# Optimization experiments

Hardware: AMD Instinct MI355X
Metric: run time of the kernel (lower is better)

The kernel has to match this reference:

```python
import jax, jax.numpy as jnp
import numpy as np

EMB_DIM = 128
HEAD_SIZE = 16  # embDim // numHea = 128 // 8


def setup_inputs() -> dict:
    key = jax.random.key(0)
    k1, k2, k3, k4 = jax.random.split(key, 4)
    B, T = 8, 2048
    inpEmb = jax.random.normal(k1, (B, T, EMB_DIM), dtype=jnp.float32)
    # nn.Linear(embDim, heaSiz, bias=False) weights, stored transposed so y = x @ W
    Wq = jax.random.normal(k2, (EMB_DIM, HEAD_SIZE), dtype=jnp.float32) / np.sqrt(EMB_DIM)
    Wk = jax.random.normal(k3, (EMB_DIM, HEAD_SIZE), dtype=jnp.float32) / np.sqrt(EMB_DIM)
    Wv = jax.random.normal(k4, (EMB_DIM, HEAD_SIZE), dtype=jnp.float32) / np.sqrt(EMB_DIM)
    return {"inpEmb": inpEmb, "Wq": Wq, "Wk": Wk, "Wv": Wv}


def reference(inpEmb, Wq, Wk, Wv):
    # q,k,v: [B, T, H]
    q = inpEmb @ Wq
    k = inpEmb @ Wk
    v = inpEmb @ Wv
    scale = HEAD_SIZE ** -0.5
    # scores: [B, T, T]
    scores = jnp.einsum('bqh,bkh->bqk', q, k) * scale
    T = inpEmb.shape[1]
    causal = jnp.tril(jnp.ones((T, T), dtype=bool))
    scores = jnp.where(causal, scores, -jnp.inf)
    weights = jax.nn.softmax(scores, axis=-1)
    # dropout treated as identity (eval mode) for deterministic reference
    return jnp.einsum('bqk,bkh->bqh', weights, v)
```

## Files before the change

### kernel.cpp

```cpp
#include <hip/hip_runtime.h>
#include <hip/hip_bf16.h>

#define T_SEQ 2048
#define EMB   128
#define H     16
#define BATCH 8
#define MAXP  16
#define QSCALE 0.360673760222241f

#define EXP2F(x) __builtin_amdgcn_exp2f(x)

typedef short short8_t __attribute__((ext_vector_type(8)));
typedef float f32x4    __attribute__((ext_vector_type(4)));

__device__ __forceinline__ unsigned short f2bf(float f) {
    __hip_bfloat16 h = __float2bfloat16(f);
    return *reinterpret_cast<unsigned short*>(&h);
}

__global__ __launch_bounds__(256) void qkv_kernel(
    const float* __restrict__ x,
    const float* __restrict__ Wq,
    const float* __restrict__ Wk,
    const float* __restrict__ Wv,
    unsigned short* __restrict__ Qbf,
    unsigned short* __restrict__ Kbf,
    unsigned short* __restrict__ Vt)
{
    __shared__ unsigned short Wt[3][16][136];

    const int tid = threadIdx.x;
#pragma unroll
    for (int p = 0; p < 6; ++p) {
        const int idx4 = tid + p * 256;
        const int flat = idx4 * 4;
        const int mm   = flat >> 11;
        const int rem  = flat & 2047;
        const int d    = rem >> 4;
        const int c0   = rem & 15;
        const float* Wm = (mm == 0) ? Wq : (mm == 1) ? Wk : Wv;
        float4 w = *reinterpret_cast<const float4*>(Wm + rem);
        Wt[mm][c0    ][d] = f2bf(w.x);
        Wt[mm][c0 + 1][d] = f2bf(w.y);
        Wt[mm][c0 + 2][d] = f2bf(w.z);
        Wt[mm][c0 + 3][d] = f2bf(w.w);
    }
    __syncthreads();

    const int wv   = tid >> 6;
    const int lane = tid & 63;
    const int q    = lane >> 4;
    const int n    = lane & 15;
    const int row0 = blockIdx.x * 64 + wv * 16;
    const float* xr = x + (size_t)(row0 + n) * EMB;

    f32x4 aq = {0,0,0,0}, ak = {0,0,0,0}, av = {0,0,0,0};
#pragma unroll
    for (int t = 0; t < 4; ++t) {
        const int k0 = t * 32 + q * 8;
        float4 xa = *reinterpret_cast<const float4*>(xr + k0);
        float4 xb = *reinterpret_cast<const float4*>(xr + k0 + 4);
        union { unsigned short s[8]; short8_t v; } xf;
        xf.s[0]=f2bf(xa.x); xf.s[1]=f2bf(xa.y); xf.s[2]=f2bf(xa.z); xf.s[3]=f2bf(xa.w);
        xf.s[4]=f2bf(xb.x); xf.s[5]=f2bf(xb.y); xf.s[6]=f2bf(xb.z); xf.s[7]=f2bf(xb.w);
        short8_t wqf = *reinterpret_cast<const short8_t*>(&Wt[0][n][k0]);
        short8_t wkf = *reinterpret_cast<const short8_t*>(&Wt[1][n][k0]);
        short8_t wvf = *reinterpret_cast<const short8_t*>(&Wt[2][n][k0]);
        aq = __builtin_amdgcn_mfma_f32_16x16x32_bf16(xf.v, wqf, aq, 0, 0, 0);
        ak = __builtin_amdgcn_mfma_f32_16x16x32_bf16(xf.v, wkf, ak, 0, 0, 0);
        av = __builtin_amdgcn_mfma_f32_16x16x32_bf16(xf.v, wvf, av, 0, 0, 0);
    }

    const int grow = row0 + q * 4;
    const int b    = grow >> 11;
    const int ib0  = grow & 2047;
#pragma unroll
    for (int r = 0; r < 4; ++r) {
        Qbf[(size_t)(grow + r) * H + n] = f2bf(aq[r] * QSCALE);
        Kbf[(size_t)(grow + r) * H + n] = f2bf(ak[r]);
    }
    union { unsigned short s[4]; unsigned long long u; } vp;
    vp.s[0]=f2bf(av[0]); vp.s[1]=f2bf(av[1]); vp.s[2]=f2bf(av[2]); vp.s[3]=f2bf(av[3]);
    *reinterpret_cast<unsigned long long*>(
        Vt + ((size_t)b * H + n) * T_SEQ + ib0) = vp.u;
}

__global__ __launch_bounds__(256) void attn_phase1(
    const unsigned short* __restrict__ Qbf,
    const unsigned short* __restrict__ Kbf,
    const unsigned short* __restrict__ Vt,
    float* __restrict__ P2)
{
    __shared__ unsigned int Pbuf[4][16][68];

    int r = blockIdx.x;
    int qt = 0;
    while (r >= (qt >> 1) + 1) { r -= (qt >> 1) + 1; ++qt; }
    const int cch  = r;
    const int b    = blockIdx.y;
    const int i0   = qt << 6;
    const int j0   = cch << 7;

    const int tid  = threadIdx.x;
    const int wv   = tid >> 6;
    const int lane = tid & 63;
    const int q    = lane >> 4;
    const int n    = lane & 15;
    const int wrow0 = i0 + wv * 16;
    const int irow  = wrow0 + n;

    const unsigned short* Qp = Qbf + (size_t)b * T_SEQ * H;
    const unsigned short* Kp = Kbf + (size_t)b * T_SEQ * H;
    const unsigned short* vrow = Vt + (size_t)b * H * T_SEQ + (size_t)n * T_SEQ;

    short8_t qf = {0,0,0,0,0,0,0,0};
    if (q < 2)
        qf = *reinterpret_cast<const short8_t*>(Qp + (size_t)irow * H + q * 8);

    f32x4 S[8];
#pragma unroll
    for (int s = 0; s < 8; ++s) {
        short8_t kf = {0,0,0,0,0,0,0,0};
        if (q < 2)
            kf = *reinterpret_cast<const short8_t*>(
                    Kp + (size_t)(j0 + s * 16 + n) * H + q * 8);
        f32x4 z = {0.f, 0.f, 0.f, 0.f};
        S[s] = __builtin_amdgcn_mfma_f32_16x16x32_bf16(kf, qf, z, 0, 0, 0);
    }
    short8_t vf[4];
#pragma unroll
    for (int h = 0; h < 4; ++h)
        vf[h] = *reinterpret_cast<const short8_t*>(vrow + j0 + h * 32 + q * 8);

    float tm = -1e30f;
    if (j0 + 127 > wrow0) {
#pragma unroll
        for (int s = 0; s < 8; ++s) {
            const int kb = j0 + s * 16 + q * 4;
#pragma unroll
            for (int rr = 0; rr < 4; ++rr) {
                float v = (kb + rr <= irow) ? S[s][rr] : -1e30f;
                S[s][rr] = v;
                tm = fmaxf(tm, v);
            }
        }
    } else {
#pragma unroll
        for (int s = 0; s < 8; ++s)
            tm = fmaxf(tm, fmaxf(fmaxf(S[s][0], S[s][1]),
                                 fmaxf(S[s][2], S[s][3])));
    }
    tm = fmaxf(tm, __shfl_xor(tm, 16));
    tm = fmaxf(tm, __shfl_xor(tm, 32));
    const float m = tm;

    float l = 0.f;
#pragma unroll
    for (int s = 0; s < 8; ++s) {
        float e0 = EXP2F(S[s][0] - m);
        float e1 = EXP2F(S[s][1] - m);
        float e2 = EXP2F(S[s][2] - m);
        float e3 = EXP2F(S[s][3] - m);
        l += (e0 + e1) + (e2 + e3);
        unsigned int b0 = __builtin_bit_cast(unsigned int, e0);
        unsigned int b1 = __builtin_bit_cast(unsigned int, e1);
        unsigned int b2 = __builtin_bit_cast(unsigned int, e2);
        unsigned int b3 = __builtin_bit_cast(unsigned int, e3);
        unsigned long long pw =
            (unsigned long long)((b1 & 0xffff0000u) | (b0 >> 16)) |
            ((unsigned long long)((b3 & 0xffff0000u) | (b2 >> 16)) << 32);
        *reinterpret_cast<unsigned long long*>(&Pbuf[wv][n][8 * s + 2 * q]) = pw;
    }

    f32x4 acc = {0.f, 0.f, 0.f, 0.f};
#pragma unroll
    for (int h = 0; h < 4; ++h) {
        uint4 p4 = *reinterpret_cast<const uint4*>(&Pbuf[wv][n][16 * h + 4 * q]);
        union { uint4 u; short8_t v; } pu; pu.u = p4;
        acc = __builtin_amdgcn_mfma_f32_16x16x32_bf16(vf[h], pu.v, acc, 0, 0, 0);
    }

    l += __shfl_xor(l, 16);
    l += __shfl_xor(l, 32);

    float* pp = P2 + ((size_t)(b * T_SEQ + irow) * MAXP + cch) * 18;
    float2 r01; r01.x = acc[0]; r01.y = acc[1];
    float2 r23; r23.x = acc[2]; r23.y = acc[3];
    *reinterpret_cast<float2*>(pp + q * 4)     = r01;
    *reinterpret_cast<float2*>(pp + q * 4 + 2) = r23;
    if (q == 0) { pp[16] = m; pp[17] = l; }
}

__global__ __launch_bounds__(256) void attn_phase2(
    const float* __restrict__ P2, float* __restrict__ out)
{
    const int gid = blockIdx.x * 256 + threadIdx.x;
    const int row = gid >> 4;
    const int d   = gid & 15;
    const int ib  = row & (T_SEQ - 1);
    const int nc  = (ib >> 7) + 1;
    const float* base = P2 + (size_t)row * (MAXP * 18);

    float M = -1e30f;
    for (int p = 0; p < nc; ++p) M = fmaxf(M, base[p * 18 + 16]);
    float L = 0.f, o = 0.f;
    for (int p = 0; p < nc; ++p) {
        const float wgt = EXP2F(base[p * 18 + 16] - M);
        L += wgt * base[p * 18 + 17];
        o += wgt * base[p * 18 + d];
    }
    out[gid] = o / L;
}

extern "C" void kernel_launch(void* const* d_in, const int* in_sizes, int n_in,
                              void* d_out, int out_size, void* d_ws, size_t ws_size,
                              hipStream_t stream)
{
    const float* x  = (const float*)d_in[0];
    const float* Wq = (const float*)d_in[1];
    const float* Wk = (const float*)d_in[2];
    const float* Wv = (const float*)d_in[3];
    float* out = (float*)d_out;

    const size_t NE = (size_t)BATCH * T_SEQ * H;
    unsigned short* Qbf = (unsigned short*)d_ws;
    unsigned short* Kbf = Qbf + NE;
    unsigned short* Vt  = Kbf + NE;
    float* P2 = (float*)(Vt + NE);

    qkv_kernel<<<BATCH * T_SEQ / 64, 256, 0, stream>>>(
        x, Wq, Wk, Wv, Qbf, Kbf, Vt);
    attn_phase1<<<dim3(272, BATCH), 256, 0, stream>>>(Qbf, Kbf, Vt, P2);
    attn_phase2<<<(int)(NE / 256), 256, 0, stream>>>(P2, out);
}
```

Measured before the change: 88.19 us.

## Fuse split-chunk attention and combine pass into one online-softmax kernel

Replaces the two-pass scheme with a single flash-style kernel. The old scheme wrote per-chunk partial outputs with their max and sum to a global buffer, then reduced them in a second launch. Now each 512-thread block owns 64 query rows, and two wave groups walk alternating key chunks with an online-softmax rescale. The two groups merge their partial results through shared memory before writing the final output. This removes the global partial-result round trip and one kernel launch. In exchange it cuts block count, serializes up to eight chunks per wave, and leaves load imbalance across query tiles. The V transpose row stride is also padded to 2064 elements.

```diff
diff --git a/kernel.cpp b/kernel.cpp
--- a/kernel.cpp
+++ b/kernel.cpp
@@ -5,7 +5,7 @@
 #define EMB   128
 #define H     16
 #define BATCH 8
-#define MAXP  16
+#define VSTR  2064
 #define QSCALE 0.360673760222241f
 
 #define EXP2F(x) __builtin_amdgcn_exp2f(x)
@@ -82,134 +82,146 @@
     union { unsigned short s[4]; unsigned long long u; } vp;
     vp.s[0]=f2bf(av[0]); vp.s[1]=f2bf(av[1]); vp.s[2]=f2bf(av[2]); vp.s[3]=f2bf(av[3]);
     *reinterpret_cast<unsigned long long*>(
-        Vt + ((size_t)b * H + n) * T_SEQ + ib0) = vp.u;
-}
-
-__global__ __launch_bounds__(256) void attn_phase1(
+        Vt + ((size_t)b * H + n) * VSTR + ib0) = vp.u;
+}
+
+__global__ __launch_bounds__(512) void attn_all(
     const unsigned short* __restrict__ Qbf,
     const unsigned short* __restrict__ Kbf,
     const unsigned short* __restrict__ Vt,
-    float* __restrict__ P2)
+    float* __restrict__ out)
 {
-    __shared__ unsigned int Pbuf[4][16][68];
-
-    int r = blockIdx.x;
-    int qt = 0;
-    while (r >= (qt >> 1) + 1) { r -= (qt >> 1) + 1; ++qt; }
-    const int cch  = r;
-    const int b    = blockIdx.y;
-    const int i0   = qt << 6;
-    const int j0   = cch << 7;
+    __shared__ unsigned int Pbuf[8][2][16][68];
+    __shared__ float Comb[4][16][18];
+
+    const int b   = blockIdx.x >> 5;
+    const int qt  = blockIdx.x & 31;
+    const int nc  = (qt >> 1) + 1;
+    const int i0  = qt << 6;
 
     const int tid  = threadIdx.x;
     const int wv   = tid >> 6;
+    const int grp  = wv >> 2;
+    const int wq   = wv & 3;
     const int lane = tid & 63;
     const int q    = lane >> 4;
     const int n    = lane & 15;
-    const int wrow0 = i0 + wv * 16;
+    const int wrow0 = i0 + wq * 16;
     const int irow  = wrow0 + n;
 
     const unsigned short* Qp = Qbf + (size_t)b * T_SEQ * H;
     const unsigned short* Kp = Kbf + (size_t)b * T_SEQ * H;
-    const unsigned short* vrow = Vt + (size_t)b * H * T_SEQ + (size_t)n * T_SEQ;
+    const unsigned short* vrow = Vt + (size_t)b * H * VSTR + (size_t)n * VSTR;
 
     short8_t qf = {0,0,0,0,0,0,0,0};
     if (q < 2)
         qf = *reinterpret_cast<const short8_t*>(Qp + (size_t)irow * H + q * 8);
 
-    f32x4 S[8];
-#pragma unroll
-    for (int s = 0; s < 8; ++s) {
-        short8_t kf = {0,0,0,0,0,0,0,0};
-        if (q < 2)
-            kf = *reinterpret_cast<const short8_t*>(
-                    Kp + (size_t)(j0 + s * 16 + n) * H + q * 8);
-        f32x4 z = {0.f, 0.f, 0.f, 0.f};
-        S[s] = __builtin_amdgcn_mfma_f32_16x16x32_bf16(kf, qf, z, 0, 0, 0);
-    }
-    short8_t vf[4];
-#pragma unroll
-    for (int h = 0; h < 4; ++h)
-        vf[h] = *reinterpret_cast<const short8_t*>(vrow + j0 + h * 32 + q * 8);
-
-    float tm = -1e30f;
-    if (j0 + 127 > wrow0) {
+    f32x4 acc = {0.f, 0.f, 0.f, 0.f};
+    float m = -1e30f, l = 0.f;
+
+    int it = 0;
+    for (int cch = grp; cch < nc; cch += 2, ++it) {
+        const int j0  = cch << 7;
+        const int par = it & 1;
+
+        f32x4 S[8];
 #pragma unroll
         for (int s = 0; s < 8; ++s) {
-            const int kb = j0 + s * 16 + q * 4;
-#pragma unroll
-            for (int rr = 0; rr < 4; ++rr) {
-                float v = (kb + rr <= irow) ? S[s][rr] : -1e30f;
-                S[s][rr] = v;
-                tm = fmaxf(tm, v);
+            short8_t kf = {0,0,0,0,0,0,0,0};
+            if (q < 2)
+                kf = *reinterpret_cast<const short8_t*>(
+                        Kp + (size_t)(j0 + s * 16 + n) * H + q * 8);
+            f32x4 z = {0.f, 0.f, 0.f, 0.f};
+            S[s] = __builtin_amdgcn_mfma_f32_16x16x32_bf16(kf, qf, z, 0, 0, 0);
+        }
+        short8_t vf[4];
+#pragma unroll
+        for (int h = 0; h < 4; ++h)
+            vf[h] = *reinterpret_cast<const short8_t*>(
+                        vrow + j0 + h * 32 + q * 8);
+
+        float tm = -1e30f;
+        if (j0 + 127 > wrow0) {
+#pragma unroll
+            for (int s = 0; s < 8; ++s) {
+                const int kb = j0 + s * 16 + q * 4;
+#pragma unroll
+                for (int rr = 0; rr < 4; ++rr) {
+                    float v = (kb + rr <= irow) ? S[s][rr] : -1e30f;
+                    S[s][rr] = v;
+                    tm = fmaxf(tm, v);
+                }
             }
-        }
-    } else {
-#pragma unroll
-        for (int s = 0; s < 8; ++s)
-            tm = fmaxf(tm, fmaxf(fmaxf(S[s][0], S[s][1]),
-                                 fmaxf(S[s][2], S[s][3])));
-    }
-    tm = fmaxf(tm, __shfl_xor(tm, 16));
-    tm = fmaxf(tm, __shfl_xor(tm, 32));
-    const float m = tm;
-
-    float l = 0.f;
-#pragma unroll
-    for (int s = 0; s < 8; ++s) {
-        float e0 = EXP2F(S[s][0] - m);
-        float e1 = EXP2F(S[s][1] - m);
-        float e2 = EXP2F(S[s][2] - m);
-        float e3 = EXP2F(S[s][3] - m);
-        l += (e0 + e1) + (e2 + e3);
-        unsigned int b0 = __builtin_bit_cast(unsigned int, e0);
-        unsigned int b1 = __builtin_bit_cast(unsigned int, e1);
-        unsigned int b2 = __builtin_bit_cast(unsigned int, e2);
-        unsigned int b3 = __builtin_bit_cast(unsigned int, e3);
-        unsigned long long pw =
-            (unsigned long long)((b1 & 0xffff0000u) | (b0 >> 16)) |
-            ((unsigned long long)((b3 & 0xffff0000u) | (b2 >> 16)) << 32);
-        *reinterpret_cast<unsigned long long*>(&Pbuf[wv][n][8 * s + 2 * q]) = pw;
-    }
-
-    f32x4 acc = {0.f, 0.f, 0.f, 0.f};
-#pragma unroll
-    for (int h = 0; h < 4; ++h) {
-        uint4 p4 = *reinterpret_cast<const uint4*>(&Pbuf[wv][n][16 * h + 4 * q]);
-        union { uint4 u; short8_t v; } pu; pu.u = p4;
-        acc = __builtin_amdgcn_mfma_f32_16x16x32_bf16(vf[h], pu.v, acc, 0, 0, 0);
+        } else {
+#pragma unroll
+            for (int s = 0; s < 8; ++s)
+                tm = fmaxf(tm, fmaxf(fmaxf(S[s][0], S[s][1]),
+                                     fmaxf(S[s][2], S[s][3])));
+        }
+        tm = fmaxf(tm, __shfl_xor(tm, 16));
+        tm = fmaxf(tm, __shfl_xor(tm, 32));
+        const float mn    = fmaxf(m, tm);
+        const float alpha = EXP2F(m - mn);
+        m = mn;
+
+        float ps = 0.f;
+#pragma unroll
+        for (int s = 0; s < 8; ++s) {
+            float e0 = EXP2F(S[s][0] - mn);
+            float e1 = EXP2F(S[s][1] - mn);
+            float e2 = EXP2F(S[s][2] - mn);
+            float e3 = EXP2F(S[s][3] - mn);
+            ps += (e0 + e1) + (e2 + e3);
+            unsigned int b0 = __builtin_bit_cast(unsigned int, e0);
+            unsigned int b1 = __builtin_bit_cast(unsigned int, e1);
+            unsigned int b2 = __builtin_bit_cast(unsigned int, e2);
+            unsigned int b3 = __builtin_bit_cast(unsigned int, e3);
+            unsigned long long pw =
+                (unsigned long long)((b1 & 0xffff0000u) | (b0 >> 16)) |
+                ((unsigned long long)((b3 & 0xffff0000u) | (b2 >> 16)) << 32);
+            *reinterpret_cast<unsigned long long*>(
+                &Pbuf[wv][par][n][8 * s + 2 * q]) = pw;
+        }
+        l = l * alpha + ps;
+        acc[0] *= alpha; acc[1] *= alpha; acc[2] *= alpha; acc[3] *= alpha;
+
+#pragma unroll
+        for (int h = 0; h < 4; ++h) {
+            uint4 p4 = *reinterpret_cast<const uint4*>(
+                    &Pbuf[wv][par][n][16 * h + 4 * q]);
+            union { uint4 u; short8_t v; } pu; pu.u = p4;
+            acc = __builtin_amdgcn_mfma_f32_16x16x32_bf16(vf[h], pu.v, acc, 0, 0, 0);
+        }
     }
 
     l += __shfl_xor(l, 16);
     l += __shfl_xor(l, 32);
 
-    float* pp = P2 + ((size_t)(b * T_SEQ + irow) * MAXP + cch) * 18;
-    float2 r01; r01.x = acc[0]; r01.y = acc[1];
-    float2 r23; r23.x = acc[2]; r23.y = acc[3];
-    *reinterpret_cast<float2*>(pp + q * 4)     = r01;
-    *reinterpret_cast<float2*>(pp + q * 4 + 2) = r23;
-    if (q == 0) { pp[16] = m; pp[17] = l; }
-}
-
-__global__ __launch_bounds__(256) void attn_phase2(
-    const float* __restrict__ P2, float* __restrict__ out)
-{
-    const int gid = blockIdx.x * 256 + threadIdx.x;
-    const int row = gid >> 4;
-    const int d   = gid & 15;
-    const int ib  = row & (T_SEQ - 1);
-    const int nc  = (ib >> 7) + 1;
-    const float* base = P2 + (size_t)row * (MAXP * 18);
-
-    float M = -1e30f;
-    for (int p = 0; p < nc; ++p) M = fmaxf(M, base[p * 18 + 16]);
-    float L = 0.f, o = 0.f;
-    for (int p = 0; p < nc; ++p) {
-        const float wgt = EXP2F(base[p * 18 + 16] - M);
-        L += wgt * base[p * 18 + 17];
-        o += wgt * base[p * 18 + d];
-    }
-    out[gid] = o / L;
+    if (grp == 1) {
+        Comb[wq][n][q * 4 + 0] = acc[0];
+        Comb[wq][n][q * 4 + 1] = acc[1];
+        Comb[wq][n][q * 4 + 2] = acc[2];
+        Comb[wq][n][q * 4 + 3] = acc[3];
+        if (q == 0) { Comb[wq][n][16] = m; Comb[wq][n][17] = l; }
+    }
+    __syncthreads();
+
+    if (grp == 0) {
+        const float m1 = Comb[wq][n][16];
+        const float l1 = Comb[wq][n][17];
+        const float M  = fmaxf(m, m1);
+        const float w0 = EXP2F(m - M);
+        const float w1 = EXP2F(m1 - M);
+        const float L  = l * w0 + l1 * w1;
+        float4 o;
+        o.x = (acc[0] * w0 + Comb[wq][n][q * 4 + 0] * w1) / L;
+        o.y = (acc[1] * w0 + Comb[wq][n][q * 4 + 1] * w1) / L;
+        o.z = (acc[2] * w0 + Comb[wq][n][q * 4 + 2] * w1) / L;
+        o.w = (acc[3] * w0 + Comb[wq][n][q * 4 + 3] * w1) / L;
+        *reinterpret_cast<float4*>(
+            out + ((size_t)(b * T_SEQ) + irow) * H + q * 4) = o;
+    }
 }
 
 extern "C" void kernel_launch(void* const* d_in, const int* in_sizes, int n_in,
@@ -226,10 +238,8 @@
     unsigned short* Qbf = (unsigned short*)d_ws;
     unsigned short* Kbf = Qbf + NE;
     unsigned short* Vt  = Kbf + NE;
-    float* P2 = (float*)(Vt + NE);
 
     qkv_kernel<<<BATCH * T_SEQ / 64, 256, 0, stream>>>(
         x, Wq, Wk, Wv, Qbf, Kbf, Vt);
-    attn_phase1<<<dim3(272, BATCH), 256, 0, stream>>>(Qbf, Kbf, Vt, P2);
-    attn_phase2<<<(int)(NE / 256), 256, 0, stream>>>(P2, out);
-}
+    attn_all<<<BATCH * 32, 512, 0, stream>>>(Qbf, Kbf, Vt, out);
+}
```

New measurement: 89.62 us. Within noise of the previous version (+1.6%).
